# Kernel tuning notes

Hardware: AMD Instinct MI355X
Metric: run time of the kernel (lower is better)

Reference implementation:

```python
import jax, jax.numpy as jnp
import numpy as np

N_NODES = 40000
N_EDGES = 640000
HIDDEN = 128
NUM_RBF = 50
CUTOFF = 10.0


def setup_inputs() -> dict:
    key = jax.random.key(0)
    ks = jax.random.split(key, 8)
    s = 1.0 / np.sqrt(HIDDEN)
    sf = 1.0 / np.sqrt(NUM_RBF)
    return {
        "x": jax.random.normal(ks[0], (N_NODES, HIDDEN), dtype=jnp.float32),
        "edge_index": jax.random.randint(ks[1], (2, N_EDGES), 0, N_NODES, dtype=jnp.int64),
        "edge_weight": jax.random.uniform(ks[2], (N_EDGES,), dtype=jnp.float32) * CUTOFF,
        "edge_attr": jax.random.normal(ks[3], (N_EDGES, NUM_RBF), dtype=jnp.float32),
        "W_f1": jax.random.normal(ks[4], (NUM_RBF, HIDDEN), dtype=jnp.float32) * sf,
        "b_f1": jnp.zeros((HIDDEN,), dtype=jnp.float32),
        "W_f2": jax.random.normal(ks[5], (HIDDEN, HIDDEN), dtype=jnp.float32) * s,
        "b_f2": jnp.zeros((HIDDEN,), dtype=jnp.float32),
        "W_in": jax.random.normal(ks[6], (HIDDEN, HIDDEN), dtype=jnp.float32) * s,
        "W_out": jax.random.normal(ks[7], (HIDDEN, HIDDEN), dtype=jnp.float32) * s,
        "b_out": jnp.zeros((HIDDEN,), dtype=jnp.float32),
        "W_lin": jax.random.normal(jax.random.fold_in(key, 7), (HIDDEN, HIDDEN), dtype=jnp.float32) * s,
        "b_lin": jnp.zeros((HIDDEN,), dtype=jnp.float32),
    }


def reference(x, edge_index, edge_weight, edge_attr,
              W_f1, b_f1, W_f2, b_f2, W_in, W_out, b_out, W_lin, b_lin):
    src = edge_index[0]
    dst = edge_index[1]
    n_nodes = x.shape[0]
    # filter network: MLP on RBF-expanded distances, modulated by cosine cutoff
    C = 0.5 * (jnp.cos(edge_weight * (jnp.pi / CUTOFF)) + 1.0)  # [E]
    Wf = jnp.tanh(edge_attr @ W_f1 + b_f1) @ W_f2 + b_f2        # [E, H]
    Wf = Wf * C[:, None]
    # cfconv: project, gather, filter-multiply, scatter-add, project
    h = x @ W_in                                                 # [N, H] (no bias)
    msg = h[src] * Wf                                            # [E, H]
    agg = jax.ops.segment_sum(msg, dst, num_segments=n_nodes)   # [N, H]
    out = agg @ W_out + b_out
    # interaction block tail: activation + linear
    out = jnp.tanh(out)
    return out @ W_lin + b_lin
```

## Files before the change

### kernel.cpp

```cpp
#include <hip/hip_runtime.h>
#include <hip/hip_bf16.h>

#define N_NODES 40000
#define N_EDGES 640000
#define HIDDEN  128
#define NUM_RBF 50
#define NBLK_SCAN 157

typedef __attribute__((ext_vector_type(8))) short bf16x8;
typedef __attribute__((ext_vector_type(4))) float f32x4;

#define WAVE_FENCE() do { asm volatile("" ::: "memory"); \
                          __builtin_amdgcn_sched_barrier(0); } while (0)

__device__ __forceinline__ short f2bf(float f) {
  __hip_bfloat16 h = __float2bfloat16(f);
  return (short)__builtin_bit_cast(unsigned short, h);
}
__device__ __forceinline__ float bf2f(unsigned short u) {
  unsigned int v = ((unsigned int)u) << 16;
  return __builtin_bit_cast(float, v);
}
__device__ __forceinline__ float bflo(unsigned int u) {
  return __builtin_bit_cast(float, u << 16);
}
__device__ __forceinline__ float bfhi(unsigned int u) {
  return __builtin_bit_cast(float, u & 0xffff0000u);
}
__device__ __forceinline__ unsigned int pack2bf(float a, float b) {
  return (unsigned int)(unsigned short)f2bf(a) |
         ((unsigned int)(unsigned short)f2bf(b) << 16);
}

__device__ __forceinline__ float fast_tanh(float x) {
  float e = __expf(2.0f * x);
  return 1.0f - 2.0f * __builtin_amdgcn_rcpf(e + 1.0f);
}

__device__ __forceinline__ f32x4 mfma16(bf16x8 a, bf16x8 b, f32x4 c) {
  return __builtin_amdgcn_mfma_f32_16x16x32_bf16(a, b, c, 0, 0, 0);
}

__device__ __forceinline__ bf16x8 load8_f32_bf16(const float* p) {
  const float4 v0 = ((const float4*)p)[0];
  const float4 v1 = ((const float4*)p)[1];
  bf16x8 r;
  r[0] = f2bf(v0.x); r[1] = f2bf(v0.y); r[2] = f2bf(v0.z); r[3] = f2bf(v0.w);
  r[4] = f2bf(v1.x); r[5] = f2bf(v1.y); r[6] = f2bf(v1.z); r[7] = f2bf(v1.w);
  return r;
}

__global__ __launch_bounds__(256) void hist_kernel(const int* __restrict__ ei,
                                                   int* __restrict__ hist) {
  int e = blockIdx.x * 256 + threadIdx.x;
  if (e < N_EDGES) atomicAdd(&hist[ei[N_EDGES + e]], 1);
}

__global__ __launch_bounds__(256) void scan1_kernel(const int* __restrict__ hist,
                                                    int* __restrict__ tmp,
                                                    int* __restrict__ bsum) {
  __shared__ int ls[256];
  const int t = threadIdx.x;
  const int i = blockIdx.x * 256 + t;
  int v = (i < N_NODES) ? hist[i] : 0;
  ls[t] = v;
  __syncthreads();
  for (int off = 1; off < 256; off <<= 1) {
    int u = (t >= off) ? ls[t - off] : 0;
    __syncthreads();
    ls[t] += u;
    __syncthreads();
  }
  if (i < N_NODES) tmp[i] = ls[t];
  if (t == 255) bsum[blockIdx.x] = ls[255];
}

__global__ __launch_bounds__(256) void scan2_kernel(const int* __restrict__ bsum,
                                                    int* __restrict__ bpfx,
                                                    int* __restrict__ row_start) {
  __shared__ int ls[256];
  const int t = threadIdx.x;
  int v = (t < NBLK_SCAN) ? bsum[t] : 0;
  ls[t] = v;
  __syncthreads();
  for (int off = 1; off < 256; off <<= 1) {
    int u = (t >= off) ? ls[t - off] : 0;
    __syncthreads();
    ls[t] += u;
    __syncthreads();
  }
  if (t < NBLK_SCAN) bpfx[t] = ls[t] - v;
  if (t == 255) row_start[N_NODES] = ls[255];
}

__global__ __launch_bounds__(256) void scan3_kernel(const int* __restrict__ hist,
                                                    const int* __restrict__ tmp,
                                                    const int* __restrict__ bpfx,
                                                    int* __restrict__ row_start,
                                                    int* __restrict__ cursor) {
  const int i = blockIdx.x * 256 + threadIdx.x;
  if (i < N_NODES) {
    int rs = tmp[i] - hist[i] + bpfx[blockIdx.x];
    row_start[i] = rs;
    cursor[i] = rs;
  }
}

__global__ __launch_bounds__(256) void perm_kernel(const int* __restrict__ ei,
                                                   int* __restrict__ cursor,
                                                   int* __restrict__ posOf) {
  int e = blockIdx.x * 256 + threadIdx.x;
  if (e < N_EDGES) {
    int dst = ei[N_EDGES + e];
    posOf[e] = atomicAdd(&cursor[dst], 1);
  }
}

__global__ __launch_bounds__(256) void hproj_kernel(
    const float* __restrict__ x, const float* __restrict__ W_in,
    unsigned short* __restrict__ hb)
{
  __shared__ __align__(16) unsigned short sWt[128 * 136];
  const int tid = threadIdx.x, wave = tid >> 6, lane = tid & 63;
  const int ln = lane & 15, grp = lane >> 4;
  const int r0 = blockIdx.x * 64;

  for (int idx = tid; idx < 128 * 128; idx += 256) {
    int k = idx >> 7, c = idx & 127;
    sWt[c * 136 + k] = f2bf(W_in[idx]);
  }
  __syncthreads();

  const size_t r = (size_t)r0 + wave * 16 + ln;
  f32x4 acc[8];
#pragma unroll
  for (int ct = 0; ct < 8; ++ct) acc[ct] = (f32x4){0.f, 0.f, 0.f, 0.f};
#pragma unroll
  for (int ks = 0; ks < 4; ++ks) {
    bf16x8 a = load8_f32_bf16(&x[r * 128 + ks * 32 + grp * 8]);
#pragma unroll
    for (int ct = 0; ct < 8; ++ct) {
      bf16x8 b = *(const bf16x8*)&sWt[(ct * 16 + ln) * 136 + ks * 32 + grp * 8];
      acc[ct] = mfma16(a, b, acc[ct]);
    }
  }
#pragma unroll
  for (int ct = 0; ct < 8; ++ct) {
#pragma unroll
    for (int i = 0; i < 4; ++i) {
      hb[(size_t)(r0 + wave * 16 + grp * 4 + i) * 128 + ct * 16 + ln] =
          (unsigned short)f2bf(acc[ct][i]);
    }
  }
}

__global__ __launch_bounds__(1024) void filt_kernel(
    const float* __restrict__ edge_attr,
    const float* __restrict__ edge_weight,
    const int*   __restrict__ ei,
    const int*   __restrict__ posOf,
    const unsigned int* __restrict__ hb32,
    const float* __restrict__ W_f1, const float* __restrict__ b_f1,
    const float* __restrict__ W_f2, const float* __restrict__ b_f2,
    unsigned int* __restrict__ msg32)
{
  __shared__ __align__(16) unsigned short sW1t[128 * 72];
  __shared__ __align__(16) unsigned short sW2t[128 * 136];
  __shared__ __align__(16) unsigned short sT[256 * 136];
  __shared__ float sb1[128], sb2[128];

  const int tid = threadIdx.x, wave = tid >> 6, lane = tid & 63;
  const int ln = lane & 15, grp = lane >> 4;

  for (int idx = tid; idx < 128 * 64; idx += 1024) {
    int k = idx >> 7, c = idx & 127;
    sW1t[c * 72 + k] = (k < NUM_RBF) ? f2bf(W_f1[k * 128 + c]) : (short)0;
  }
  for (int idx = tid; idx < 128 * 128; idx += 1024) {
    int k = idx >> 7, c = idx & 127;
    sW2t[c * 136 + k] = f2bf(W_f2[idx]);
  }
  if (tid < 128) { sb1[tid] = b_f1[tid]; sb2[tid] = b_f2[tid]; }
  __syncthreads();

  const int gw = blockIdx.x * 16 + wave;
  const int nw = gridDim.x * 16;
  const int nChunks = N_EDGES / 16;

  for (int chunk = gw; chunk < nChunks; chunk += nw) {
    const int e0 = chunk * 16;

    int pos[16];
    unsigned int hv[16];
#pragma unroll
    for (int j = 0; j < 16; ++j) {
      int e = e0 + j;
      int src = ei[e];
      pos[j] = posOf[e];
      hv[j] = hb32[(size_t)src * 64 + lane];
    }

    const float* ap = edge_attr + (size_t)(e0 + ln) * NUM_RBF;
    bf16x8 a0, a1;
    {
      const float2* p = (const float2*)(ap + grp * 8);
      float2 v0 = p[0], v1 = p[1], v2 = p[2], v3 = p[3];
      a0[0] = f2bf(v0.x); a0[1] = f2bf(v0.y); a0[2] = f2bf(v1.x); a0[3] = f2bf(v1.y);
      a0[4] = f2bf(v2.x); a0[5] = f2bf(v2.y); a0[6] = f2bf(v3.x); a0[7] = f2bf(v3.y);
    }
    a1 = (bf16x8){0, 0, 0, 0, 0, 0, 0, 0};
    if (grp < 2) {
      const float2* p = (const float2*)(ap + 32 + grp * 8);
      float2 v0 = p[0], v1 = p[1], v2 = p[2], v3 = p[3];
      a1[0] = f2bf(v0.x); a1[1] = f2bf(v0.y); a1[2] = f2bf(v1.x); a1[3] = f2bf(v1.y);
      a1[4] = f2bf(v2.x); a1[5] = f2bf(v2.y); a1[6] = f2bf(v3.x); a1[7] = f2bf(v3.y);
    } else if (grp == 2) {
      const float2* p = (const float2*)(ap + 48);
      float2 v0 = p[0];
      a1[0] = f2bf(v0.x); a1[1] = f2bf(v0.y);
    }

#pragma unroll
    for (int ct = 0; ct < 8; ++ct) {
      f32x4 z = {0.f, 0.f, 0.f, 0.f};
      int c = ct * 16 + ln;
      bf16x8 b0 = *(const bf16x8*)&sW1t[c * 72 + grp * 8];
      bf16x8 b1 = *(const bf16x8*)&sW1t[c * 72 + 32 + grp * 8];
      z = mfma16(a0, b0, z);
      z = mfma16(a1, b1, z);
      float bias = sb1[c];
#pragma unroll
      for (int i = 0; i < 4; ++i) {
        int rl = wave * 16 + grp * 4 + i;
        sT[rl * 136 + c] = (unsigned short)f2bf(fast_tanh(z[i] + bias));
      }
    }
    WAVE_FENCE();

    bf16x8 af[4];
#pragma unroll
    for (int ks = 0; ks < 4; ++ks)
      af[ks] = *(const bf16x8*)&sT[(wave * 16 + ln) * 136 + ks * 32 + grp * 8];
    WAVE_FENCE();
    float Cv[4];
#pragma unroll
    for (int i = 0; i < 4; ++i)
      Cv[i] = 0.5f * (__cosf(edge_weight[e0 + grp * 4 + i] * 0.31415926535f) + 1.0f);
#pragma unroll
    for (int ct = 0; ct < 8; ++ct) {
      f32x4 z = {0.f, 0.f, 0.f, 0.f};
      int c = ct * 16 + ln;
#pragma unroll
      for (int ks = 0; ks < 4; ++ks) {
        bf16x8 b = *(const bf16x8*)&sW2t[c * 136 + ks * 32 + grp * 8];
        z = mfma16(af[ks], b, z);
      }
      float bias = sb2[c];
#pragma unroll
      for (int i = 0; i < 4; ++i) {
        int rl = wave * 16 + grp * 4 + i;
        sT[rl * 136 + c] = (unsigned short)f2bf((z[i] + bias) * Cv[i]);
      }
    }
    WAVE_FENCE();

#pragma unroll
    for (int j = 0; j < 16; ++j) {
      unsigned int w = *(const unsigned int*)&sT[(wave * 16 + j) * 136 + lane * 2];
      msg32[(size_t)pos[j] * 64 + lane] =
          pack2bf(bflo(w) * bflo(hv[j]), bfhi(w) * bfhi(hv[j]));
    }
    WAVE_FENCE();
  }
}

__global__ __launch_bounds__(256) void segsum_kernel(
    const int* __restrict__ row_start,
    const unsigned int* __restrict__ msg32,
    float* __restrict__ aggf)
{
  const int node = blockIdx.x * 4 + (threadIdx.x >> 6);
  const int lane = threadIdx.x & 63;
  const int eb = row_start[node], ee = row_start[node + 1];
  const int n = ee - eb;
  const unsigned int* p = msg32 + (size_t)eb * 64 + lane;
  float ax = 0.f, ay = 0.f, bx = 0.f, by = 0.f;
  int k = 0;
  for (; k + 1 < n; k += 2) {
    unsigned int u0 = p[(size_t)k * 64];
    unsigned int u1 = p[(size_t)(k + 1) * 64];
    ax += bflo(u0); ay += bfhi(u0);
    bx += bflo(u1); by += bfhi(u1);
  }
  if (k < n) {
    unsigned int u0 = p[(size_t)k * 64];
    ax += bflo(u0); ay += bfhi(u0);
  }
  ((float2*)aggf)[(size_t)node * 64 + lane] = make_float2(ax + bx, ay + by);
}

__global__ __launch_bounds__(256) void tail_kernel(
    const float* agg,
    const float* __restrict__ W_out, const float* __restrict__ b_out,
    const float* __restrict__ W_lin, const float* __restrict__ b_lin,
    float* out)
{
  __shared__ __align__(16) unsigned short sWo[128 * 136];
  __shared__ __align__(16) unsigned short sWl[128 * 136];
  __shared__ __align__(16) unsigned short sT[64 * 136];
  __shared__ float sbo[128], sbl[128];
  const int tid = threadIdx.x, wave = tid >> 6, lane = tid & 63;
  const int ln = lane & 15, grp = lane >> 4;
  const int r0 = blockIdx.x * 64;

  for (int idx = tid; idx < 128 * 128; idx += 256) {
    int k = idx >> 7, c = idx & 127;
    sWo[c * 136 + k] = f2bf(W_out[idx]);
    sWl[c * 136 + k] = f2bf(W_lin[idx]);
  }
  if (tid < 128) { sbo[tid] = b_out[tid]; sbl[tid] = b_lin[tid]; }
  __syncthreads();

  const size_t r = (size_t)r0 + wave * 16 + ln;
  f32x4 acc[8];
#pragma unroll
  for (int ct = 0; ct < 8; ++ct) acc[ct] = (f32x4){0.f, 0.f, 0.f, 0.f};
#pragma unroll
  for (int ks = 0; ks < 4; ++ks) {
    bf16x8 a = load8_f32_bf16(&agg[r * 128 + ks * 32 + grp * 8]);
#pragma unroll
    for (int ct = 0; ct < 8; ++ct) {
      bf16x8 b = *(const bf16x8*)&sWo[(ct * 16 + ln) * 136 + ks * 32 + grp * 8];
      acc[ct] = mfma16(a, b, acc[ct]);
    }
  }
#pragma unroll
  for (int ct = 0; ct < 8; ++ct) {
    int c = ct * 16 + ln;
    float bias = sbo[c];
#pragma unroll
    for (int i = 0; i < 4; ++i) {
      int rl = wave * 16 + grp * 4 + i;
      sT[rl * 136 + c] = f2bf(fast_tanh(acc[ct][i] + bias));
    }
  }
  __syncthreads();

  bf16x8 af[4];
#pragma unroll
  for (int ks = 0; ks < 4; ++ks)
    af[ks] = *(const bf16x8*)&sT[(wave * 16 + ln) * 136 + ks * 32 + grp * 8];
  f32x4 acc2[8];
#pragma unroll
  for (int ct = 0; ct < 8; ++ct) {
    f32x4 z = {0.f, 0.f, 0.f, 0.f};
    int c = ct * 16 + ln;
#pragma unroll
    for (int ks = 0; ks < 4; ++ks) {
      bf16x8 b = *(const bf16x8*)&sWl[c * 136 + ks * 32 + grp * 8];
      z = mfma16(af[ks], b, z);
    }
    acc2[ct] = z;
  }
  __syncthreads();
#pragma unroll
  for (int ct = 0; ct < 8; ++ct) {
    int c = ct * 16 + ln;
    float bias = sbl[c];
#pragma unroll
    for (int i = 0; i < 4; ++i) {
      out[(size_t)(r0 + wave * 16 + grp * 4 + i) * 128 + c] = acc2[ct][i] + bias;
    }
  }
}

__global__ __launch_bounds__(256, 2) void edge_kernel(
    const float* __restrict__ edge_attr,
    const int*   __restrict__ edge_index,
    const float* __restrict__ edge_weight,
    const float* __restrict__ W_f1, const float* __restrict__ b_f1,
    const float* __restrict__ W_f2, const float* __restrict__ b_f2,
    const unsigned short* __restrict__ hb, float* __restrict__ agg)
{
  __shared__ __align__(16) unsigned short sW1t[128 * 72];
  __shared__ __align__(16) unsigned short sW2t[128 * 136];
  __shared__ __align__(16) unsigned short sT[64 * 136];
  __shared__ float sb1[128], sb2[128], sC[64];
  __shared__ int sSrc[64], sDst[64];

  const int tid = threadIdx.x, wave = tid >> 6, lane = tid & 63;
  const int ln = lane & 15, grp = lane >> 4;

  for (int idx = tid; idx < 128 * 64; idx += 256) {
    int k = idx >> 7, c = idx & 127;
    sW1t[c * 72 + k] = (k < NUM_RBF) ? f2bf(W_f1[k * 128 + c]) : (short)0;
  }
  for (int idx = tid; idx < 128 * 128; idx += 256) {
    int k = idx >> 7, c = idx & 127;
    sW2t[c * 136 + k] = f2bf(W_f2[idx]);
  }
  if (tid < 128) { sb1[tid] = b_f1[tid]; sb2[tid] = b_f2[tid]; }

  const int nTiles = N_EDGES / 64;
  for (int tile = blockIdx.x; tile < nTiles; tile += gridDim.x) {
    const int e0 = tile * 64;
    for (int idx = tid; idx < 64 * NUM_RBF; idx += 256) {
      int e = idx / NUM_RBF, k = idx - e * NUM_RBF;
      sT[e * 136 + k] = f2bf(edge_attr[(size_t)e0 * NUM_RBF + idx]);
    }
    for (int idx = tid; idx < 64 * 14; idx += 256) {
      int e = idx / 14, k = NUM_RBF + (idx - (idx / 14) * 14);
      sT[e * 136 + k] = 0;
    }
    if (tid < 64) {
      int e = e0 + tid;
      sC[tid] = 0.5f * (__cosf(edge_weight[e] * 0.31415926535f) + 1.0f);
      sSrc[tid] = edge_index[e];
      sDst[tid] = edge_index[N_EDGES + e];
    }
    __syncthreads();

    const int erow = wave * 16 + ln;
    bf16x8 a0 = *(const bf16x8*)&sT[erow * 136 + grp * 8];
    bf16x8 a1 = *(const bf16x8*)&sT[erow * 136 + 32 + grp * 8];
    __syncthreads();

    f32x4 acc[8];
#pragma unroll
    for (int ct = 0; ct < 8; ++ct) {
      f32x4 z = {0.f, 0.f, 0.f, 0.f};
      int c = ct * 16 + ln;
      bf16x8 b0 = *(const bf16x8*)&sW1t[c * 72 + grp * 8];
      bf16x8 b1 = *(const bf16x8*)&sW1t[c * 72 + 32 + grp * 8];
      z = mfma16(a0, b0, z);
      z = mfma16(a1, b1, z);
      acc[ct] = z;
    }
#pragma unroll
    for (int ct = 0; ct < 8; ++ct) {
      int c = ct * 16 + ln;
      float bias = sb1[c];
#pragma unroll
      for (int i = 0; i < 4; ++i) {
        int el = wave * 16 + grp * 4 + i;
        sT[el * 136 + c] = f2bf(fast_tanh(acc[ct][i] + bias));
      }
    }
    __syncthreads();

    bf16x8 af[4];
#pragma unroll
    for (int ks = 0; ks < 4; ++ks)
      af[ks] = *(const bf16x8*)&sT[erow * 136 + ks * 32 + grp * 8];
    f32x4 acc2[8];
#pragma unroll
    for (int ct = 0; ct < 8; ++ct) {
      f32x4 z = {0.f, 0.f, 0.f, 0.f};
      int c = ct * 16 + ln;
#pragma unroll
      for (int ks = 0; ks < 4; ++ks) {
        bf16x8 b = *(const bf16x8*)&sW2t[c * 136 + ks * 32 + grp * 8];
        z = mfma16(af[ks], b, z);
      }
      acc2[ct] = z;
    }
#pragma unroll
    for (int ct = 0; ct < 8; ++ct) {
      int c = ct * 16 + ln;
      float bias = sb2[c];
#pragma unroll
      for (int i = 0; i < 4; ++i) {
        int el = wave * 16 + grp * 4 + i;
        float wf = (acc2[ct][i] + bias) * sC[el];
        float m = bf2f(hb[(size_t)sSrc[el] * 128 + c]) * wf;
        atomicAdd(&agg[(size_t)sDst[el] * 128 + c], m);
      }
    }
    __syncthreads();
  }
}

extern "C" void kernel_launch(void* const* d_in, const int* in_sizes, int n_in,
                              void* d_out, int out_size, void* d_ws, size_t ws_size,
                              hipStream_t stream) {
  const float* x     = (const float*)d_in[0];
  const int*   ei    = (const int*)d_in[1];
  const float* ew    = (const float*)d_in[2];
  const float* ea    = (const float*)d_in[3];
  const float* W_f1  = (const float*)d_in[4];
  const float* b_f1  = (const float*)d_in[5];
  const float* W_f2  = (const float*)d_in[6];
  const float* b_f2  = (const float*)d_in[7];
  const float* W_in  = (const float*)d_in[8];
  const float* W_out = (const float*)d_in[9];
  const float* b_out = (const float*)d_in[10];
  const float* W_lin = (const float*)d_in[11];
  const float* b_lin = (const float*)d_in[12];

  const size_t HB_B  = (size_t)N_NODES * HIDDEN * 2;
  const size_t MSG_B = (size_t)N_EDGES * HIDDEN * 2;
  const size_t I_B   = (size_t)N_NODES * 4;
  const size_t RS_B  = ((size_t)(N_NODES + 1) * 4 + 15) & ~(size_t)15;
  const size_t SB_B  = 1024;
  const size_t POS_B = (size_t)N_EDGES * 4;
  const size_t NEED = HB_B + MSG_B + I_B + RS_B + I_B + I_B + SB_B + SB_B + POS_B;

  char* ws = (char*)d_ws;
  unsigned short* hb = (unsigned short*)ws;

  if (ws_size >= NEED) {
    char* q = ws + HB_B;
    unsigned short* msg = (unsigned short*)q;  q += MSG_B;
    int* hist      = (int*)q;                  q += I_B;
    int* row_start = (int*)q;                  q += RS_B;
    int* cursor    = (int*)q;                  q += I_B;
    int* tmp       = (int*)q;                  q += I_B;
    int* bsum      = (int*)q;                  q += SB_B;
    int* bpfx      = (int*)q;                  q += SB_B;
    int* posOf     = (int*)q;

    hipMemsetAsync(hist, 0, I_B, stream);
    hist_kernel<<<(N_EDGES + 255) / 256, 256, 0, stream>>>(ei, hist);
    scan1_kernel<<<NBLK_SCAN, 256, 0, stream>>>(hist, tmp, bsum);
    scan2_kernel<<<1, 256, 0, stream>>>(bsum, bpfx, row_start);
    scan3_kernel<<<NBLK_SCAN, 256, 0, stream>>>(hist, tmp, bpfx, row_start, cursor);
    perm_kernel<<<(N_EDGES + 255) / 256, 256, 0, stream>>>(ei, cursor, posOf);
    hproj_kernel<<<N_NODES / 64, 256, 0, stream>>>(x, W_in, hb);
    filt_kernel<<<256, 1024, 0, stream>>>(ea, ew, ei, posOf,
                                          (const unsigned int*)hb,
                                          W_f1, b_f1, W_f2, b_f2,
                                          (unsigned int*)msg);
    segsum_kernel<<<N_NODES / 4, 256, 0, stream>>>(row_start,
                                                   (const unsigned int*)msg,
                                                   (float*)d_out);
    tail_kernel<<<N_NODES / 64, 256, 0, stream>>>((const float*)d_out,
                                                  W_out, b_out, W_lin, b_lin,
                                                  (float*)d_out);
  } else {
    float* agg = (float*)(ws + HB_B);
    hipMemsetAsync(agg, 0, (size_t)N_NODES * HIDDEN * 4, stream);
    hproj_kernel<<<N_NODES / 64, 256, 0, stream>>>(x, W_in, hb);
    edge_kernel<<<512, 256, 0, stream>>>(ea, ei, ew, W_f1, b_f1, W_f2, b_f2, hb, agg);
    tail_kernel<<<N_NODES / 64, 256, 0, stream>>>(agg, W_out, b_out, W_lin, b_lin,
                                                  (float*)d_out);
  }
}
```

Before: 239.2 us.

## Fuse filter MLP with CSR segment-sum, dropping materialized message buffer

The perm kernel now writes a dst-sorted list of (edge id, src) pairs, and a new fused kernel has each wave walk groups of 4 destination nodes in CSR order. For each 16-edge tile it computes the filter MLP, multiplies by the gathered h[src] and cutoff, and accumulates directly into per-node registers. This removes the write and re-read of the E×128 bf16 message buffer and one kernel launch. In exchange, edge_attr and edge_weight reads become indirect gathers, and tiles are partly wasted at group boundaries and tails.

```diff
diff --git a/kernel.cpp b/kernel.cpp
--- a/kernel.cpp
+++ b/kernel.cpp
@@ -108,11 +108,12 @@
 
 __global__ __launch_bounds__(256) void perm_kernel(const int* __restrict__ ei,
                                                    int* __restrict__ cursor,
-                                                   int* __restrict__ posOf) {
+                                                   int2* __restrict__ epk) {
   int e = blockIdx.x * 256 + threadIdx.x;
   if (e < N_EDGES) {
     int dst = ei[N_EDGES + e];
-    posOf[e] = atomicAdd(&cursor[dst], 1);
+    int pos = atomicAdd(&cursor[dst], 1);
+    epk[pos] = make_int2(e, ei[e]);
   }
 }
 
@@ -154,15 +155,15 @@
   }
 }
 
-__global__ __launch_bounds__(1024) void filt_kernel(
+__global__ __launch_bounds__(1024) void edgeagg_kernel(
     const float* __restrict__ edge_attr,
     const float* __restrict__ edge_weight,
-    const int*   __restrict__ ei,
-    const int*   __restrict__ posOf,
+    const int*  __restrict__ row_start,
+    const int2* __restrict__ epk,
     const unsigned int* __restrict__ hb32,
     const float* __restrict__ W_f1, const float* __restrict__ b_f1,
     const float* __restrict__ W_f2, const float* __restrict__ b_f2,
-    unsigned int* __restrict__ msg32)
+    float* __restrict__ aggf)
 {
   __shared__ __align__(16) unsigned short sW1t[128 * 72];
   __shared__ __align__(16) unsigned short sW2t[128 * 136];
@@ -185,118 +186,119 @@
 
   const int gw = blockIdx.x * 16 + wave;
   const int nw = gridDim.x * 16;
-  const int nChunks = N_EDGES / 16;
-
-  for (int chunk = gw; chunk < nChunks; chunk += nw) {
-    const int e0 = chunk * 16;
-
-    int pos[16];
-    unsigned int hv[16];
-#pragma unroll
-    for (int j = 0; j < 16; ++j) {
-      int e = e0 + j;
-      int src = ei[e];
-      pos[j] = posOf[e];
-      hv[j] = hb32[(size_t)src * 64 + lane];
-    }
-
-    const float* ap = edge_attr + (size_t)(e0 + ln) * NUM_RBF;
-    bf16x8 a0, a1;
-    {
-      const float2* p = (const float2*)(ap + grp * 8);
-      float2 v0 = p[0], v1 = p[1], v2 = p[2], v3 = p[3];
-      a0[0] = f2bf(v0.x); a0[1] = f2bf(v0.y); a0[2] = f2bf(v1.x); a0[3] = f2bf(v1.y);
-      a0[4] = f2bf(v2.x); a0[5] = f2bf(v2.y); a0[6] = f2bf(v3.x); a0[7] = f2bf(v3.y);
-    }
-    a1 = (bf16x8){0, 0, 0, 0, 0, 0, 0, 0};
-    if (grp < 2) {
-      const float2* p = (const float2*)(ap + 32 + grp * 8);
-      float2 v0 = p[0], v1 = p[1], v2 = p[2], v3 = p[3];
-      a1[0] = f2bf(v0.x); a1[1] = f2bf(v0.y); a1[2] = f2bf(v1.x); a1[3] = f2bf(v1.y);
-      a1[4] = f2bf(v2.x); a1[5] = f2bf(v2.y); a1[6] = f2bf(v3.x); a1[7] = f2bf(v3.y);
-    } else if (grp == 2) {
-      const float2* p = (const float2*)(ap + 48);
-      float2 v0 = p[0];
-      a1[0] = f2bf(v0.x); a1[1] = f2bf(v0.y);
-    }
-
-#pragma unroll
-    for (int ct = 0; ct < 8; ++ct) {
-      f32x4 z = {0.f, 0.f, 0.f, 0.f};
-      int c = ct * 16 + ln;
-      bf16x8 b0 = *(const bf16x8*)&sW1t[c * 72 + grp * 8];
-      bf16x8 b1 = *(const bf16x8*)&sW1t[c * 72 + 32 + grp * 8];
-      z = mfma16(a0, b0, z);
-      z = mfma16(a1, b1, z);
-      float bias = sb1[c];
-#pragma unroll
-      for (int i = 0; i < 4; ++i) {
-        int rl = wave * 16 + grp * 4 + i;
-        sT[rl * 136 + c] = (unsigned short)f2bf(fast_tanh(z[i] + bias));
-      }
-    }
-    WAVE_FENCE();
-
-    bf16x8 af[4];
-#pragma unroll
-    for (int ks = 0; ks < 4; ++ks)
-      af[ks] = *(const bf16x8*)&sT[(wave * 16 + ln) * 136 + ks * 32 + grp * 8];
-    WAVE_FENCE();
-    float Cv[4];
-#pragma unroll
-    for (int i = 0; i < 4; ++i)
-      Cv[i] = 0.5f * (__cosf(edge_weight[e0 + grp * 4 + i] * 0.31415926535f) + 1.0f);
-#pragma unroll
-    for (int ct = 0; ct < 8; ++ct) {
-      f32x4 z = {0.f, 0.f, 0.f, 0.f};
-      int c = ct * 16 + ln;
-#pragma unroll
-      for (int ks = 0; ks < 4; ++ks) {
-        bf16x8 b = *(const bf16x8*)&sW2t[c * 136 + ks * 32 + grp * 8];
-        z = mfma16(af[ks], b, z);
-      }
-      float bias = sb2[c];
-#pragma unroll
-      for (int i = 0; i < 4; ++i) {
-        int rl = wave * 16 + grp * 4 + i;
-        sT[rl * 136 + c] = (unsigned short)f2bf((z[i] + bias) * Cv[i]);
-      }
-    }
-    WAVE_FENCE();
-
-#pragma unroll
-    for (int j = 0; j < 16; ++j) {
-      unsigned int w = *(const unsigned int*)&sT[(wave * 16 + j) * 136 + lane * 2];
-      msg32[(size_t)pos[j] * 64 + lane] =
-          pack2bf(bflo(w) * bflo(hv[j]), bfhi(w) * bfhi(hv[j]));
-    }
-    WAVE_FENCE();
-  }
-}
-
-__global__ __launch_bounds__(256) void segsum_kernel(
-    const int* __restrict__ row_start,
-    const unsigned int* __restrict__ msg32,
-    float* __restrict__ aggf)
-{
-  const int node = blockIdx.x * 4 + (threadIdx.x >> 6);
-  const int lane = threadIdx.x & 63;
-  const int eb = row_start[node], ee = row_start[node + 1];
-  const int n = ee - eb;
-  const unsigned int* p = msg32 + (size_t)eb * 64 + lane;
-  float ax = 0.f, ay = 0.f, bx = 0.f, by = 0.f;
-  int k = 0;
-  for (; k + 1 < n; k += 2) {
-    unsigned int u0 = p[(size_t)k * 64];
-    unsigned int u1 = p[(size_t)(k + 1) * 64];
-    ax += bflo(u0); ay += bfhi(u0);
-    bx += bflo(u1); by += bfhi(u1);
-  }
-  if (k < n) {
-    unsigned int u0 = p[(size_t)k * 64];
-    ax += bflo(u0); ay += bfhi(u0);
-  }
-  ((float2*)aggf)[(size_t)node * 64 + lane] = make_float2(ax + bx, ay + by);
+  const int nGroups = N_NODES / 4;
+
+  for (int ng = gw; ng < nGroups; ng += nw) {
+    const int n0 = ng * 4;
+    const int rs0 = row_start[n0],     rs1 = row_start[n0 + 1];
+    const int rs2 = row_start[n0 + 2], rs3 = row_start[n0 + 3];
+    const int rs4 = row_start[n0 + 4];
+
+    float ax = 0.f, ay = 0.f;
+    int cur = 0;
+    int nb = rs1;
+
+    for (int gb = rs0; gb < rs4; gb += 16) {
+      const int lim = (rs4 - gb < 16) ? (rs4 - gb) : 16;
+
+      unsigned int hv[16];
+#pragma unroll
+      for (int j = 0; j < 16; ++j) {
+        int s = gb + j; if (s >= rs4) s = rs4 - 1;
+        int src = epk[s].y;
+        hv[j] = hb32[(size_t)src * 64 + lane];
+      }
+
+      int sl = gb + ln; if (sl >= rs4) sl = rs4 - 1;
+      const int eA = epk[sl].x;
+      const float Cw =
+          0.5f * (__cosf(edge_weight[eA] * 0.31415926535f) + 1.0f);
+
+      const float* ap = edge_attr + (size_t)eA * NUM_RBF;
+      bf16x8 a0, a1;
+      {
+        const float2* p = (const float2*)(ap + grp * 8);
+        float2 v0 = p[0], v1 = p[1], v2 = p[2], v3 = p[3];
+        a0[0] = f2bf(v0.x); a0[1] = f2bf(v0.y); a0[2] = f2bf(v1.x); a0[3] = f2bf(v1.y);
+        a0[4] = f2bf(v2.x); a0[5] = f2bf(v2.y); a0[6] = f2bf(v3.x); a0[7] = f2bf(v3.y);
+      }
+      a1 = (bf16x8){0, 0, 0, 0, 0, 0, 0, 0};
+      if (grp < 2) {
+        const float2* p = (const float2*)(ap + 32 + grp * 8);
+        float2 v0 = p[0], v1 = p[1], v2 = p[2], v3 = p[3];
+        a1[0] = f2bf(v0.x); a1[1] = f2bf(v0.y); a1[2] = f2bf(v1.x); a1[3] = f2bf(v1.y);
+        a1[4] = f2bf(v2.x); a1[5] = f2bf(v2.y); a1[6] = f2bf(v3.x); a1[7] = f2bf(v3.y);
+      } else if (grp == 2) {
+        const float2* p = (const float2*)(ap + 48);
+        float2 v0 = p[0];
+        a1[0] = f2bf(v0.x); a1[1] = f2bf(v0.y);
+      }
+
+#pragma unroll
+      for (int ct = 0; ct < 8; ++ct) {
+        f32x4 z = {0.f, 0.f, 0.f, 0.f};
+        int c = ct * 16 + ln;
+        bf16x8 b0 = *(const bf16x8*)&sW1t[c * 72 + grp * 8];
+        bf16x8 b1 = *(const bf16x8*)&sW1t[c * 72 + 32 + grp * 8];
+        z = mfma16(a0, b0, z);
+        z = mfma16(a1, b1, z);
+        float bias = sb1[c];
+#pragma unroll
+        for (int i = 0; i < 4; ++i) {
+          int rl = wave * 16 + grp * 4 + i;
+          sT[rl * 136 + c] = (unsigned short)f2bf(fast_tanh(z[i] + bias));
+        }
+      }
+      WAVE_FENCE();
+
+      bf16x8 af[4];
+#pragma unroll
+      for (int ks = 0; ks < 4; ++ks)
+        af[ks] = *(const bf16x8*)&sT[(wave * 16 + ln) * 136 + ks * 32 + grp * 8];
+      WAVE_FENCE();
+#pragma unroll
+      for (int ct = 0; ct < 8; ++ct) {
+        f32x4 z = {0.f, 0.f, 0.f, 0.f};
+        int c = ct * 16 + ln;
+#pragma unroll
+        for (int ks = 0; ks < 4; ++ks) {
+          bf16x8 b = *(const bf16x8*)&sW2t[c * 136 + ks * 32 + grp * 8];
+          z = mfma16(af[ks], b, z);
+        }
+        float bias = sb2[c];
+#pragma unroll
+        for (int i = 0; i < 4; ++i) {
+          int rl = wave * 16 + grp * 4 + i;
+          sT[rl * 136 + c] = (unsigned short)f2bf(z[i] + bias);
+        }
+      }
+      WAVE_FENCE();
+
+#pragma unroll
+      for (int j = 0; j < 16; ++j) {
+        if (j < lim) {
+          while (cur < 4 && gb + j == nb) {
+            ((float2*)aggf)[(size_t)(n0 + cur) * 64 + lane] =
+                make_float2(ax, ay);
+            ax = 0.f; ay = 0.f;
+            ++cur;
+            nb = (cur == 1) ? rs2 : (cur == 2) ? rs3 : rs4;
+          }
+          unsigned int w = *(const unsigned int*)&sT[(wave * 16 + j) * 136 + lane * 2];
+          float C = __shfl(Cw, j, 64);
+          ax = fmaf(C * bflo(w), bflo(hv[j]), ax);
+          ay = fmaf(C * bfhi(w), bfhi(hv[j]), ay);
+        }
+      }
+      WAVE_FENCE();
+    }
+
+    while (cur < 4) {
+      ((float2*)aggf)[(size_t)(n0 + cur) * 64 + lane] = make_float2(ax, ay);
+      ax = 0.f; ay = 0.f;
+      ++cur;
+    }
+  }
 }
 
 __global__ __launch_bounds__(256) void tail_kernel(
@@ -498,41 +500,36 @@
   const float* b_lin = (const float*)d_in[12];
 
   const size_t HB_B  = (size_t)N_NODES * HIDDEN * 2;
-  const size_t MSG_B = (size_t)N_EDGES * HIDDEN * 2;
   const size_t I_B   = (size_t)N_NODES * 4;
   const size_t RS_B  = ((size_t)(N_NODES + 1) * 4 + 15) & ~(size_t)15;
   const size_t SB_B  = 1024;
-  const size_t POS_B = (size_t)N_EDGES * 4;
-  const size_t NEED = HB_B + MSG_B + I_B + RS_B + I_B + I_B + SB_B + SB_B + POS_B;
+  const size_t EPK_B = (size_t)N_EDGES * 8;
+  const size_t NEED = HB_B + I_B + RS_B + I_B + I_B + SB_B + SB_B + EPK_B;
 
   char* ws = (char*)d_ws;
   unsigned short* hb = (unsigned short*)ws;
 
   if (ws_size >= NEED) {
     char* q = ws + HB_B;
-    unsigned short* msg = (unsigned short*)q;  q += MSG_B;
     int* hist      = (int*)q;                  q += I_B;
     int* row_start = (int*)q;                  q += RS_B;
     int* cursor    = (int*)q;                  q += I_B;
     int* tmp       = (int*)q;                  q += I_B;
     int* bsum      = (int*)q;                  q += SB_B;
     int* bpfx      = (int*)q;                  q += SB_B;
-    int* posOf     = (int*)q;
+    int2* epk      = (int2*)q;
 
     hipMemsetAsync(hist, 0, I_B, stream);
     hist_kernel<<<(N_EDGES + 255) / 256, 256, 0, stream>>>(ei, hist);
     scan1_kernel<<<NBLK_SCAN, 256, 0, stream>>>(hist, tmp, bsum);
     scan2_kernel<<<1, 256, 0, stream>>>(bsum, bpfx, row_start);
     scan3_kernel<<<NBLK_SCAN, 256, 0, stream>>>(hist, tmp, bpfx, row_start, cursor);
-    perm_kernel<<<(N_EDGES + 255) / 256, 256, 0, stream>>>(ei, cursor, posOf);
+    perm_kernel<<<(N_EDGES + 255) / 256, 256, 0, stream>>>(ei, cursor, epk);
     hproj_kernel<<<N_NODES / 64, 256, 0, stream>>>(x, W_in, hb);
-    filt_kernel<<<256, 1024, 0, stream>>>(ea, ew, ei, posOf,
-                                          (const unsigned int*)hb,
-                                          W_f1, b_f1, W_f2, b_f2,
-                                          (unsigned int*)msg);
-    segsum_kernel<<<N_NODES / 4, 256, 0, stream>>>(row_start,
-                                                   (const unsigned int*)msg,
-                                                   (float*)d_out);
+    edgeagg_kernel<<<256, 1024, 0, stream>>>(ea, ew, row_start, epk,
+                                             (const unsigned int*)hb,
+                                             W_f1, b_f1, W_f2, b_f2,
+                                             (float*)d_out);
     tail_kernel<<<N_NODES / 64, 256, 0, stream>>>((const float*)d_out,
                                                   W_out, b_out, W_lin, b_lin,
                                                   (float*)d_out);
```

After: 226.2 us. 5.5% less time.
